# Kernel optimization log

Measured on AMD Instinct MI355X. Metric: run time of the kernel, lower is better.

The kernel has to match this reference:

```python
import jax, jax.numpy as jnp
import numpy as np

N_NODES = 100000


def _gcn_norm(edge_index, num_nodes):
    # add self loops
    loops = jnp.arange(num_nodes, dtype=edge_index.dtype)
    row = jnp.concatenate([edge_index[0], loops])  # source
    col = jnp.concatenate([edge_index[1], loops])  # target
    ones = jnp.ones(row.shape[0], dtype=jnp.float32)
    deg = jax.ops.segment_sum(ones, col, num_segments=num_nodes)
    dinv = jnp.where(deg > 0, jax.lax.rsqrt(deg), 0.0)
    norm = dinv[row] * dinv[col]  # [E + N]
    return row, col, norm


def reference(x, edge_index, weight, bias):
    num_nodes = x.shape[0]
    row, col, norm = _gcn_norm(edge_index, num_nodes)
    # K = 2 hops of D^-1/2 (A + I) D^-1/2 propagation
    for _ in range(2):
        msgs = x[row] * norm[:, None]                      # [E+N, F] gather
        x = jax.ops.segment_sum(msgs, col, num_segments=num_nodes)  # scatter-add
    logits = x @ weight + bias                              # [N, classes]
    return jax.nn.log_softmax(logits, axis=1)


def setup_inputs() -> dict:
    key = jax.random.key(0)
    k1, k2, k3 = jax.random.split(key, 3)
    x = jax.random.normal(k1, (N_NODES, 128), dtype=jnp.float32)
    edge_index = jax.random.randint(k2, (2, 1600000), 0, N_NODES, dtype=jnp.int64)
    weight = jax.random.normal(k3, (128, 40), dtype=jnp.float32) * (1.0 / np.sqrt(128.0))
    bias = jnp.zeros((40,), dtype=jnp.float32)
    return {"x": x, "edge_index": edge_index, "weight": weight, "bias": bias}
```

## Files before the change

### kernel.cpp

```cpp
#include <hip/hip_runtime.h>
#include <math.h>

#define NN 100000
#define F_IN 128
#define F_OUT 40
#define BSHIFT 9
#define BSIZE (1 << BSHIFT)
#define NBUCK ((NN + BSIZE - 1) >> BSHIFT)
#define SCAP 12288
#define CAP 14336
#define EPB_C 4096
#define OFFB  ((unsigned)((NN + 1) * 64))
#define ADUM  ((unsigned)(NN * 64))
#define XSBYTES ((size_t)8000128)

typedef short bf16x8 __attribute__((ext_vector_type(8)));
typedef float f32x4 __attribute__((ext_vector_type(4)));
typedef _Float16 h2 __attribute__((ext_vector_type(2)));

union U4H { uint4 u; h2 h[4]; };

__device__ __forceinline__ short f2bf(float f) {
    union { float f; unsigned u; } uf; uf.f = f;
    unsigned r = uf.u + 0x7FFF + ((uf.u >> 16) & 1);
    return (short)(r >> 16);
}

__device__ __forceinline__ unsigned pack16(float x, float y) {
    union { _Float16 h; unsigned short s; } a, b;
    a.h = (_Float16)x; b.h = (_Float16)y;
    return (unsigned)a.s | ((unsigned)b.s << 16);
}

__device__ __forceinline__ h2 shfl_h2(h2 v, int src) {
    int x = __builtin_bit_cast(int, v);
    x = __shfl(x, src);
    return __builtin_bit_cast(h2, x);
}

__global__ void setup_kernel(int* __restrict__ bcursor, char* xs1, char* xs2) {
    int t = threadIdx.x;
    if (t < NBUCK) bcursor[t * 16] = t * SCAP;
    if (t < 16)      *(unsigned*)(xs1 + ADUM + t * 4) = 0u;
    else if (t < 20) *(unsigned*)(xs1 + OFFB + (size_t)NN * 16 + (t - 16) * 4) = 0u;
    else if (t < 36) *(unsigned*)(xs2 + ADUM + (t - 20) * 4) = 0u;
    else if (t < 40) *(unsigned*)(xs2 + OFFB + (size_t)NN * 16 + (t - 36) * 4) = 0u;
}

__global__ void __launch_bounds__(512) part_kernel(const int* __restrict__ row,
                                                   const int* __restrict__ col,
                                                   int* __restrict__ bcursor,
                                                   int* __restrict__ staged, int E) {
    __shared__ int h[NBUCK];
    __shared__ int cur[NBUCK];
    int t = threadIdx.x;
    for (int i = t; i < NBUCK; i += 512) h[i] = 0;
    __syncthreads();
    int e0 = blockIdx.x * EPB_C;
    int ne = min(EPB_C, E - e0);
    int nq = ne >> 2;
    const int4* c4 = (const int4*)(col + e0);
    const int4* r4 = (const int4*)(row + e0);
    for (int k = t; k < nq; k += 512) {
        int4 c = c4[k];
        atomicAdd(&h[c.x >> BSHIFT], 1);
        atomicAdd(&h[c.y >> BSHIFT], 1);
        atomicAdd(&h[c.z >> BSHIFT], 1);
        atomicAdd(&h[c.w >> BSHIFT], 1);
    }
    __syncthreads();
    for (int i = t; i < NBUCK; i += 512)
        cur[i] = h[i] ? atomicAdd(&bcursor[i * 16], h[i]) : 0;
    __syncthreads();
    for (int k = t; k < nq; k += 512) {
        int4 c = c4[k];
        int4 r = r4[k];
        int p;
        p = atomicAdd(&cur[c.x >> BSHIFT], 1); staged[p] = ((c.x & 511) << 17) | r.x;
        p = atomicAdd(&cur[c.y >> BSHIFT], 1); staged[p] = ((c.y & 511) << 17) | r.y;
        p = atomicAdd(&cur[c.z >> BSHIFT], 1); staged[p] = ((c.z & 511) << 17) | r.z;
        p = atomicAdd(&cur[c.w >> BSHIFT], 1); staged[p] = ((c.w & 511) << 17) | r.w;
    }
}

__global__ void __launch_bounds__(512) build_kernel(const int* __restrict__ staged,
                                                    const int* __restrict__ bcursor,
                                                    int* __restrict__ adj,
                                                    int* __restrict__ offs,
                                                    float* __restrict__ dinv, int N) {
    __shared__ int hist[BSIZE];
    __shared__ int cur[BSIZE];
    __shared__ int wsum[8];
    int bk = blockIdx.x;
    int node0 = bk << BSHIFT;
    int sbase = bk * SCAP;
    int count = bcursor[bk * 16] - sbase;
    int gbase = bk * CAP;
    int i = threadIdx.x;
    hist[i] = 0;
    __syncthreads();
    int nq = count >> 2;
    const int4* st4 = (const int4*)(staged + sbase);
    for (int k = i; k < nq; k += 512) {
        int4 s = st4[k];
        atomicAdd(&hist[s.x >> 17], 1);
        atomicAdd(&hist[s.y >> 17], 1);
        atomicAdd(&hist[s.z >> 17], 1);
        atomicAdd(&hist[s.w >> 17], 1);
    }
    int tb = sbase + (nq << 2);
    if (i < (count & 3)) atomicAdd(&hist[staged[tb + i] >> 17], 1);
    __syncthreads();
    int v = hist[i];
    int Lp = ((v + 3) / 3) * 3;
    int L1 = max(Lp, __shfl_xor(Lp, 1));
    int LL = max(L1, __shfl_xor(L1, 2));
    int lane = i & 63, w = i >> 6;
    int x = LL;
#pragma unroll
    for (int d = 1; d < 64; d <<= 1) {
        int y = __shfl_up(x, d, 64);
        if (lane >= d) x += y;
    }
    if (lane == 63) wsum[w] = x;
    __syncthreads();
    int wpre = 0;
    for (int k = 0; k < w; ++k) wpre += wsum[k];
    int excl = wpre + x - LL;
    int n = node0 + i;
    if (n < N) {
        offs[n] = gbase + excl;
        dinv[n] = rsqrtf((float)v + 1.0f);
        adj[gbase + excl] = n;
        for (int p = excl + 1 + v; p < excl + LL; ++p)
            adj[gbase + p] = NN;
    }
    cur[i] = excl + 1;
    __syncthreads();
    for (int k = i; k < nq; k += 512) {
        int4 s = st4[k];
        int p;
        p = atomicAdd(&cur[s.x >> 17], 1); adj[gbase + p] = s.x & 0x1FFFF;
        p = atomicAdd(&cur[s.y >> 17], 1); adj[gbase + p] = s.y & 0x1FFFF;
        p = atomicAdd(&cur[s.z >> 17], 1); adj[gbase + p] = s.z & 0x1FFFF;
        p = atomicAdd(&cur[s.w >> 17], 1); adj[gbase + p] = s.w & 0x1FFFF;
    }
    if (i < (count & 3)) {
        int sv = staged[tb + i];
        int p = atomicAdd(&cur[sv >> 17], 1);
        adj[gbase + p] = sv & 0x1FFFF;
    }
}

__global__ void __launch_bounds__(256) gemm_kernel(const float* __restrict__ x,
                                                   const float* __restrict__ w,
                                                   const float* __restrict__ dinv,
                                                   char* __restrict__ xsb, int N) {
    __shared__ bf16x8 shB[3][4][64];
    int t = threadIdx.x;
    for (int idx = t; idx < 3 * 4 * 64; idx += 256) {
        int lane = idx & 63;
        int ks = (idx >> 6) & 3;
        int jt = idx >> 8;
        int j = 16 * jt + (lane & 15);
        int k0 = 32 * ks + 8 * (lane >> 4);
        bf16x8 v;
#pragma unroll
        for (int i = 0; i < 8; ++i)
            v[i] = (j < F_OUT) ? f2bf(w[(k0 + i) * F_OUT + j]) : (short)0;
        shB[jt][ks][lane] = v;
    }
    __syncthreads();
    int wave = t >> 6, lane = t & 63;
    int node0 = blockIdx.x * 64 + wave * 16;
    if (node0 >= N) return;

    const float* xrow = x + (size_t)(node0 + (lane & 15)) * F_IN + 8 * (lane >> 4);
    f32x4 acc0 = {0.f, 0.f, 0.f, 0.f};
    f32x4 acc1 = acc0, acc2 = acc0;
#pragma unroll
    for (int ks = 0; ks < 4; ++ks) {
        float4 lo = *(const float4*)(xrow + 32 * ks);
        float4 hi = *(const float4*)(xrow + 32 * ks + 4);
        bf16x8 a;
        a[0] = f2bf(lo.x); a[1] = f2bf(lo.y); a[2] = f2bf(lo.z); a[3] = f2bf(lo.w);
        a[4] = f2bf(hi.x); a[5] = f2bf(hi.y); a[6] = f2bf(hi.z); a[7] = f2bf(hi.w);
        acc0 = __builtin_amdgcn_mfma_f32_16x16x32_bf16(a, shB[0][ks][lane], acc0, 0, 0, 0);
        acc1 = __builtin_amdgcn_mfma_f32_16x16x32_bf16(a, shB[1][ks][lane], acc1, 0, 0, 0);
        acc2 = __builtin_amdgcn_mfma_f32_16x16x32_bf16(a, shB[2][ks][lane], acc2, 0, 0, 0);
    }
    int colj = lane & 15;
    int rbase = (lane >> 4) * 4;
#pragma unroll
    for (int r = 0; r < 4; ++r) {
        int node = node0 + rbase + r;
        float d = dinv[node];
        _Float16* dstA = (_Float16*)(xsb + (size_t)node * 64);
        dstA[colj]      = (_Float16)(acc0[r] * d);
        dstA[16 + colj] = (_Float16)(acc1[r] * d);
        if (colj < 8)
            ((_Float16*)(xsb + OFFB + (size_t)node * 16))[colj] = (_Float16)(acc2[r] * d);
    }
}

template <int HOP2>
__global__ void __launch_bounds__(256) hop_kernel(const int* __restrict__ offs,
                                                  const float* __restrict__ dinv,
                                                  const int* __restrict__ adj,
                                                  const char* __restrict__ src,
                                                  char* __restrict__ dst,
                                                  const float* __restrict__ bias,
                                                  float* __restrict__ out) {
    int t = threadIdx.x;
    int wave = t >> 6, lane = t & 63;
    int n0 = blockIdx.x * 16 + wave * 4;
    int node = lane >> 4;
    int sub = lane & 15;
    int n = n0 + node;
    int s = sub / 5;
    int q = sub - s * 5;
    bool padl = (sub == 15);
    unsigned strideB = padl ? 0u : (q == 4 ? 16u : 64u);
    unsigned cstB    = padl ? ADUM : (q == 4 ? OFFB : (unsigned)(q * 16));

    int obase = offs[n];
    int L = offs[n0 + 1] - offs[n0];
    int nj = L / 3;

    h2 A0 = {0.f, 0.f}, A1 = A0, A2 = A0, A3 = A0;
#define ACC4(qq) do { A0 += qq.h[0]; A1 += qq.h[1]; A2 += qq.h[2]; A3 += qq.h[3]; } while (0)

    int r = adj[obase + s];
    U4H cur; cur.u = *(const uint4*)(src + (unsigned)r * strideB + cstB);
    for (int j = 1; j < nj; ++j) {
        int r2 = adj[obase + j * 3 + s];
        U4H nxt; nxt.u = *(const uint4*)(src + (unsigned)r2 * strideB + cstB);
        ACC4(cur);
        cur = nxt;
    }
    ACC4(cur);
#undef ACC4

    int nb = lane & 0x30;
    int i1 = nb | ((sub + 5) % 15);
    int i2 = nb | ((sub + 10) % 15);
    A0 = A0 + shfl_h2(A0, i1) + shfl_h2(A0, i2);
    A1 = A1 + shfl_h2(A1, i1) + shfl_h2(A1, i2);
    A2 = A2 + shfl_h2(A2, i1) + shfl_h2(A2, i2);
    A3 = A3 + shfl_h2(A3, i1) + shfl_h2(A3, i2);

    float f0 = (float)A0[0], f1 = (float)A0[1];
    float f2 = (float)A1[0], f3 = (float)A1[1];
    float f4 = (float)A2[0], f5 = (float)A2[1];
    float f6 = (float)A3[0], f7 = (float)A3[1];

    if (!HOP2) {
        if (sub < 5) {
            float d = dinv[n];
            float dd = d * d;
            uint4 wv;
            wv.x = pack16(f0 * dd, f1 * dd);
            wv.y = pack16(f2 * dd, f3 * dd);
            wv.z = pack16(f4 * dd, f5 * dd);
            wv.w = pack16(f6 * dd, f7 * dd);
            *(uint4*)(dst + (unsigned)n * strideB + cstB) = wv;
        }
    } else {
        float d = dinv[n];
        float4 b0 = ((const float4*)bias)[2 * q];
        float4 b1 = ((const float4*)bias)[2 * q + 1];
        float l0 = f0 * d + b0.x, l1 = f1 * d + b0.y;
        float l2 = f2 * d + b0.z, l3 = f3 * d + b0.w;
        float l4 = f4 * d + b1.x, l5 = f5 * d + b1.y;
        float l6 = f6 * d + b1.z, l7 = f7 * d + b1.w;
        float mp = fmaxf(fmaxf(fmaxf(l0, l1), fmaxf(l2, l3)),
                         fmaxf(fmaxf(l4, l5), fmaxf(l6, l7)));
        float m = mp;
#pragma unroll
        for (int dd = 1; dd <= 4; ++dd)
            m = fmaxf(m, __shfl(mp, nb | ((sub + dd) % 5)));
        const float R = 1.44269504089f;
        float sp = exp2f((l0 - m) * R) + exp2f((l1 - m) * R)
                 + exp2f((l2 - m) * R) + exp2f((l3 - m) * R)
                 + exp2f((l4 - m) * R) + exp2f((l5 - m) * R)
                 + exp2f((l6 - m) * R) + exp2f((l7 - m) * R);
        float sx = sp;
#pragma unroll
        for (int dd = 1; dd <= 4; ++dd)
            sx += __shfl(sp, nb | ((sub + dd) % 5));
        if (sub < 5) {
            float ls = m + 0.69314718056f * log2f(sx);
            float4 q0 = {l0 - ls, l1 - ls, l2 - ls, l3 - ls};
            float4 q1 = {l4 - ls, l5 - ls, l6 - ls, l7 - ls};
            float* op = out + (size_t)n * F_OUT + 8 * q;
            *(float4*)op = q0;
            *(float4*)(op + 4) = q1;
        }
    }
}

extern "C" void kernel_launch(void* const* d_in, const int* in_sizes, int n_in,
                              void* d_out, int out_size, void* d_ws, size_t ws_size,
                              hipStream_t stream) {
    const float* x    = (const float*)d_in[0];
    const int*   eidx = (const int*)d_in[1];
    const float* w    = (const float*)d_in[2];
    const float* bias = (const float*)d_in[3];
    float* out = (float*)d_out;

    const int E = in_sizes[1] / 2;
    const int N = NN;

    char* ws = (char*)d_ws;
    int*   bcursor = (int*)ws;   ws += 4096 * 4;
    int*   offs    = (int*)ws;   ws += (size_t)N * 4;
    float* dinv    = (float*)ws; ws += (size_t)N * 4;
    int*   adj     = (int*)ws;   ws += (size_t)NBUCK * CAP * 4;
    char*  xs1     = ws;         ws += XSBYTES;
    char*  xs2     = ws;         ws += XSBYTES;
    int*   staged  = (int*)ws;

    const int* row = eidx;
    const int* col = eidx + E;

    setup_kernel<<<1, 256, 0, stream>>>(bcursor, xs1, xs2);
    part_kernel<<<(E + EPB_C - 1) / EPB_C, 512, 0, stream>>>(row, col, bcursor, staged, E);
    build_kernel<<<NBUCK, 512, 0, stream>>>(staged, bcursor, adj, offs, dinv, N);

    gemm_kernel<<<(N + 63) / 64, 256, 0, stream>>>(x, w, dinv, xs1, N);

    hop_kernel<0><<<N / 16, 256, 0, stream>>>(offs, dinv, adj, xs1, xs2, bias, out);
    hop_kernel<1><<<N / 16, 256, 0, stream>>>(offs, dinv, adj, xs2, nullptr, bias, out);
}
```

Measured before the change: 124.5 us.

## Fuse GEMM into CSR build kernel and fold setup into partition kernel

Removes the separate setup and gemm kernels. Bucket cursors become relative counts zeroed by a memset, and the padding zeroing moves into block 0 of the partition kernel. Each build block then runs the bf16 MFMA projection for its 512 nodes, using dinv held in shared memory. This saves launches and a dinv reload, but it runs the x-streaming GEMM on far fewer blocks, which may reduce memory-level parallelism.

Result: faster. 117.4 us (-5.7%).

```diff
diff --git a/kernel.cpp b/kernel.cpp
--- a/kernel.cpp
+++ b/kernel.cpp
@@ -38,22 +38,21 @@
     return __builtin_bit_cast(h2, x);
 }
 
-__global__ void setup_kernel(int* __restrict__ bcursor, char* xs1, char* xs2) {
-    int t = threadIdx.x;
-    if (t < NBUCK) bcursor[t * 16] = t * SCAP;
-    if (t < 16)      *(unsigned*)(xs1 + ADUM + t * 4) = 0u;
-    else if (t < 20) *(unsigned*)(xs1 + OFFB + (size_t)NN * 16 + (t - 16) * 4) = 0u;
-    else if (t < 36) *(unsigned*)(xs2 + ADUM + (t - 20) * 4) = 0u;
-    else if (t < 40) *(unsigned*)(xs2 + OFFB + (size_t)NN * 16 + (t - 36) * 4) = 0u;
-}
-
 __global__ void __launch_bounds__(512) part_kernel(const int* __restrict__ row,
                                                    const int* __restrict__ col,
                                                    int* __restrict__ bcursor,
-                                                   int* __restrict__ staged, int E) {
+                                                   int* __restrict__ staged,
+                                                   char* __restrict__ xs1,
+                                                   char* __restrict__ xs2, int E) {
     __shared__ int h[NBUCK];
     __shared__ int cur[NBUCK];
     int t = threadIdx.x;
+    if (blockIdx.x == 0) {
+        if (t < 16)      *(unsigned*)(xs1 + ADUM + t * 4) = 0u;
+        else if (t < 20) *(unsigned*)(xs1 + OFFB + (size_t)NN * 16 + (t - 16) * 4) = 0u;
+        else if (t < 36) *(unsigned*)(xs2 + ADUM + (t - 20) * 4) = 0u;
+        else if (t < 40) *(unsigned*)(xs2 + OFFB + (size_t)NN * 16 + (t - 36) * 4) = 0u;
+    }
     for (int i = t; i < NBUCK; i += 512) h[i] = 0;
     __syncthreads();
     int e0 = blockIdx.x * EPB_C;
@@ -70,7 +69,7 @@
     }
     __syncthreads();
     for (int i = t; i < NBUCK; i += 512)
-        cur[i] = h[i] ? atomicAdd(&bcursor[i * 16], h[i]) : 0;
+        cur[i] = (h[i] ? atomicAdd(&bcursor[i * 16], h[i]) : 0) + i * SCAP;
     __syncthreads();
     for (int k = t; k < nq; k += 512) {
         int4 c = c4[k];
@@ -87,16 +86,33 @@
                                                     const int* __restrict__ bcursor,
                                                     int* __restrict__ adj,
                                                     int* __restrict__ offs,
-                                                    float* __restrict__ dinv, int N) {
+                                                    float* __restrict__ dinv,
+                                                    const float* __restrict__ x,
+                                                    const float* __restrict__ w,
+                                                    char* __restrict__ xsb, int N) {
     __shared__ int hist[BSIZE];
     __shared__ int cur[BSIZE];
     __shared__ int wsum[8];
+    __shared__ float sdinv[BSIZE];
+    __shared__ bf16x8 shB[3][4][64];
     int bk = blockIdx.x;
     int node0 = bk << BSHIFT;
     int sbase = bk * SCAP;
-    int count = bcursor[bk * 16] - sbase;
+    int count = bcursor[bk * 16];
     int gbase = bk * CAP;
     int i = threadIdx.x;
+    for (int idx = i; idx < 3 * 4 * 64; idx += 512) {
+        int lane = idx & 63;
+        int ks = (idx >> 6) & 3;
+        int jt = idx >> 8;
+        int j = 16 * jt + (lane & 15);
+        int k0 = 32 * ks + 8 * (lane >> 4);
+        bf16x8 v;
+#pragma unroll
+        for (int ii = 0; ii < 8; ++ii)
+            v[ii] = (j < F_OUT) ? f2bf(w[(k0 + ii) * F_OUT + j]) : (short)0;
+        shB[jt][ks][lane] = v;
+    }
     hist[i] = 0;
     __syncthreads();
     int nq = count >> 2;
@@ -115,22 +131,24 @@
     int Lp = ((v + 3) / 3) * 3;
     int L1 = max(Lp, __shfl_xor(Lp, 1));
     int LL = max(L1, __shfl_xor(L1, 2));
-    int lane = i & 63, w = i >> 6;
-    int x = LL;
+    int lane = i & 63, wv = i >> 6;
+    int xsc = LL;
 #pragma unroll
     for (int d = 1; d < 64; d <<= 1) {
-        int y = __shfl_up(x, d, 64);
-        if (lane >= d) x += y;
-    }
-    if (lane == 63) wsum[w] = x;
+        int y = __shfl_up(xsc, d, 64);
+        if (lane >= d) xsc += y;
+    }
+    if (lane == 63) wsum[wv] = xsc;
     __syncthreads();
     int wpre = 0;
-    for (int k = 0; k < w; ++k) wpre += wsum[k];
-    int excl = wpre + x - LL;
+    for (int k = 0; k < wv; ++k) wpre += wsum[k];
+    int excl = wpre + xsc - LL;
     int n = node0 + i;
+    float dv = rsqrtf((float)v + 1.0f);
+    sdinv[i] = dv;
     if (n < N) {
         offs[n] = gbase + excl;
-        dinv[n] = rsqrtf((float)v + 1.0f);
+        dinv[n] = dv;
         adj[gbase + excl] = n;
         for (int p = excl + 1 + v; p < excl + LL; ++p)
             adj[gbase + p] = NN;
@@ -150,56 +168,39 @@
         int p = atomicAdd(&cur[sv >> 17], 1);
         adj[gbase + p] = sv & 0x1FFFF;
     }
-}
-
-__global__ void __launch_bounds__(256) gemm_kernel(const float* __restrict__ x,
-                                                   const float* __restrict__ w,
-                                                   const float* __restrict__ dinv,
-                                                   char* __restrict__ xsb, int N) {
-    __shared__ bf16x8 shB[3][4][64];
-    int t = threadIdx.x;
-    for (int idx = t; idx < 3 * 4 * 64; idx += 256) {
-        int lane = idx & 63;
-        int ks = (idx >> 6) & 3;
-        int jt = idx >> 8;
-        int j = 16 * jt + (lane & 15);
-        int k0 = 32 * ks + 8 * (lane >> 4);
-        bf16x8 v;
-#pragma unroll
-        for (int i = 0; i < 8; ++i)
-            v[i] = (j < F_OUT) ? f2bf(w[(k0 + i) * F_OUT + j]) : (short)0;
-        shB[jt][ks][lane] = v;
-    }
-    __syncthreads();
-    int wave = t >> 6, lane = t & 63;
-    int node0 = blockIdx.x * 64 + wave * 16;
-    if (node0 >= N) return;
-
-    const float* xrow = x + (size_t)(node0 + (lane & 15)) * F_IN + 8 * (lane >> 4);
-    f32x4 acc0 = {0.f, 0.f, 0.f, 0.f};
-    f32x4 acc1 = acc0, acc2 = acc0;
-#pragma unroll
-    for (int ks = 0; ks < 4; ++ks) {
-        float4 lo = *(const float4*)(xrow + 32 * ks);
-        float4 hi = *(const float4*)(xrow + 32 * ks + 4);
-        bf16x8 a;
-        a[0] = f2bf(lo.x); a[1] = f2bf(lo.y); a[2] = f2bf(lo.z); a[3] = f2bf(lo.w);
-        a[4] = f2bf(hi.x); a[5] = f2bf(hi.y); a[6] = f2bf(hi.z); a[7] = f2bf(hi.w);
-        acc0 = __builtin_amdgcn_mfma_f32_16x16x32_bf16(a, shB[0][ks][lane], acc0, 0, 0, 0);
-        acc1 = __builtin_amdgcn_mfma_f32_16x16x32_bf16(a, shB[1][ks][lane], acc1, 0, 0, 0);
-        acc2 = __builtin_amdgcn_mfma_f32_16x16x32_bf16(a, shB[2][ks][lane], acc2, 0, 0, 0);
-    }
-    int colj = lane & 15;
-    int rbase = (lane >> 4) * 4;
-#pragma unroll
-    for (int r = 0; r < 4; ++r) {
-        int node = node0 + rbase + r;
-        float d = dinv[node];
-        _Float16* dstA = (_Float16*)(xsb + (size_t)node * 64);
-        dstA[colj]      = (_Float16)(acc0[r] * d);
-        dstA[16 + colj] = (_Float16)(acc1[r] * d);
-        if (colj < 8)
-            ((_Float16*)(xsb + OFFB + (size_t)node * 16))[colj] = (_Float16)(acc2[r] * d);
+
+    int wave = i >> 6;
+    int lane6 = i & 63;
+    int colj = lane6 & 15;
+    int rbase = (lane6 >> 4) * 4;
+#pragma unroll
+    for (int g = 0; g < 4; ++g) {
+        int node0g = node0 + g * 128 + wave * 16;
+        if (node0g >= N) break;
+        const float* xrow = x + (size_t)(node0g + colj) * F_IN + 8 * (lane6 >> 4);
+        f32x4 acc0 = {0.f, 0.f, 0.f, 0.f};
+        f32x4 acc1 = acc0, acc2 = acc0;
+#pragma unroll
+        for (int ks = 0; ks < 4; ++ks) {
+            float4 lo = *(const float4*)(xrow + 32 * ks);
+            float4 hi = *(const float4*)(xrow + 32 * ks + 4);
+            bf16x8 a;
+            a[0] = f2bf(lo.x); a[1] = f2bf(lo.y); a[2] = f2bf(lo.z); a[3] = f2bf(lo.w);
+            a[4] = f2bf(hi.x); a[5] = f2bf(hi.y); a[6] = f2bf(hi.z); a[7] = f2bf(hi.w);
+            acc0 = __builtin_amdgcn_mfma_f32_16x16x32_bf16(a, shB[0][ks][lane6], acc0, 0, 0, 0);
+            acc1 = __builtin_amdgcn_mfma_f32_16x16x32_bf16(a, shB[1][ks][lane6], acc1, 0, 0, 0);
+            acc2 = __builtin_amdgcn_mfma_f32_16x16x32_bf16(a, shB[2][ks][lane6], acc2, 0, 0, 0);
+        }
+#pragma unroll
+        for (int r = 0; r < 4; ++r) {
+            int node = node0g + rbase + r;
+            float d = sdinv[node - node0];
+            _Float16* dstA = (_Float16*)(xsb + (size_t)node * 64);
+            dstA[colj]      = (_Float16)(acc0[r] * d);
+            dstA[16 + colj] = (_Float16)(acc1[r] * d);
+            if (colj < 8)
+                ((_Float16*)(xsb + OFFB + (size_t)node * 16))[colj] = (_Float16)(acc2[r] * d);
+        }
     }
 }
 
@@ -323,11 +324,11 @@
     const int* row = eidx;
     const int* col = eidx + E;
 
-    setup_kernel<<<1, 256, 0, stream>>>(bcursor, xs1, xs2);
-    part_kernel<<<(E + EPB_C - 1) / EPB_C, 512, 0, stream>>>(row, col, bcursor, staged, E);
-    build_kernel<<<NBUCK, 512, 0, stream>>>(staged, bcursor, adj, offs, dinv, N);
-
-    gemm_kernel<<<(N + 63) / 64, 256, 0, stream>>>(x, w, dinv, xs1, N);
+    hipMemsetAsync(bcursor, 0, 4096 * 4, stream);
+    part_kernel<<<(E + EPB_C - 1) / EPB_C, 512, 0, stream>>>(row, col, bcursor, staged,
+                                                             xs1, xs2, E);
+    build_kernel<<<NBUCK, 512, 0, stream>>>(staged, bcursor, adj, offs, dinv,
+                                            x, w, xs1, N);
 
     hop_kernel<0><<<N / 16, 256, 0, stream>>>(offs, dinv, adj, xs1, xs2, bias, out);
     hop_kernel<1><<<N / 16, 256, 0, stream>>>(offs, dinv, adj, xs2, nullptr, bias, out);
```
